# Kernel optimization log

Measured on AMD Instinct MI355X. Metric: run time of the kernel, lower is better.

Reference implementation:

```python
import jax, jax.numpy as jnp
import numpy as np

BL = 5           # block_len
BS = BL * BL     # block_size = 25
NH = 8           # num_heads
MASK_ONES = 12   # first 12 window positions unmasked (causal raster mask)


def _rel_pos_index():
    coords = np.stack(np.meshgrid(np.arange(BL), np.arange(BL), indexing='ij')).reshape(2, -1)
    rel = coords[:, :, None] - coords[:, None, :]          # [2, 25, 25]
    idx = (rel[0] + BL - 1) * (2 * BL - 1) + (rel[1] + BL - 1)
    return idx                                              # [25, 25] int

_REL_IDX = _rel_pos_index()


def _layernorm(x, w, b, eps=1e-5):
    m = jnp.mean(x, axis=-1, keepdims=True)
    v = jnp.var(x, axis=-1, keepdims=True)
    return (x - m) * jax.lax.rsqrt(v + eps) * w + b


def setup_inputs() -> dict:
    key = jax.random.key(0)
    ks = jax.random.split(key, 16)
    B, C, H, W = 4, 64, 64, 64
    out_dim = 64
    hidden = int(C * 4.0)
    s = lambda k, shape, scale=0.02: jax.random.normal(k, shape, dtype=jnp.float32) * scale
    return {
        'x': jax.random.normal(ks[0], (B, C, H, W), dtype=jnp.float32),
        'norm1_w': jnp.ones((C,), jnp.float32), 'norm1_b': jnp.zeros((C,), jnp.float32),
        'qkv_w': s(ks[1], (3 * C, C)), 'qkv_b': s(ks[2], (3 * C,)),
        'rpb_table': s(ks[3], ((2 * BL - 1) * (2 * BL - 1), NH)),
        'norm2_w': jnp.ones((C,), jnp.float32), 'norm2_b': jnp.zeros((C,), jnp.float32),
        'fc1_w': s(ks[4], (hidden, C)), 'fc1_b': s(ks[5], (hidden,)),
        'fc2_w': s(ks[6], (C, hidden)), 'fc2_b': s(ks[7], (C,)),
        'proj_w': s(ks[8], (out_dim, C)), 'proj_b': s(ks[9], (out_dim,)),
    }


def reference(x, norm1_w, norm1_b, qkv_w, qkv_b, rpb_table,
              norm2_w, norm2_b, fc1_w, fc1_b, fc2_w, fc2_b, proj_w, proj_b):
    B, C, H, W = x.shape
    hd = C // NH
    scale = hd ** (-0.5)

    # F.unfold(kernel=5, pad=2): per-pixel 5x5 neighborhood, channel-major then (kh,kw)
    xp = jnp.pad(x, ((0, 0), (0, 0), (2, 2), (2, 2)))
    patches = jnp.stack([xp[:, :, i:i + H, j:j + W] for i in range(BL) for j in range(BL)], axis=2)  # [B,C,25,H,W]
    x_unfold = patches.reshape(B, C, BS, H * W).transpose(0, 3, 2, 1)  # [B,HW,25,C]

    mask = (jnp.arange(BS) < MASK_ONES).astype(x.dtype)[None, None, :, None]
    x_masked = x_unfold * mask

    out = _layernorm(x_masked, norm1_w, norm1_b)
    qkv = out @ qkv_w.T + qkv_b                                 # [B,HW,25,3C]
    qkv = qkv.reshape(B, H * W, BS, 3, NH, hd).transpose(3, 0, 1, 4, 2, 5)  # [3,B,HW,nh,25,hd]
    q, k, v = qkv[0] * scale, qkv[1], qkv[2]

    attn = jnp.einsum('bpnqd,bpnkd->bpnqk', q, k)               # [B,HW,nh,25,25]
    bias = rpb_table[_REL_IDX.reshape(-1)].reshape(BS, BS, NH).transpose(2, 0, 1)  # [nh,25,25]
    attn = jax.nn.softmax(attn + bias[None, None], axis=-1)

    o = jnp.einsum('bpnqk,bpnkd->bpnqd', attn, v)               # [B,HW,nh,25,hd]
    o = o.transpose(0, 1, 3, 2, 4).reshape(B, H * W, BS, C)
    o = o + x_masked
    out_sumed = jnp.sum(o, axis=2)                              # [B,HW,C]

    y = _layernorm(out_sumed, norm2_w, norm2_b)
    y = jax.nn.gelu(y @ fc1_w.T + fc1_b, approximate=False) @ fc2_w.T + fc2_b
    y = y + out_sumed
    y = y @ proj_w.T + proj_b                                   # [B,HW,out_dim]
    return y.reshape(B, H, W, -1).transpose(0, 3, 1, 2)
```

## Files before the change

### kernel.cpp

```cpp
#include <hip/hip_runtime.h>
#include <hip/hip_bf16.h>


typedef _Float16 h2f __attribute__((ext_vector_type(2)));
typedef _Float16 h8  __attribute__((ext_vector_type(8)));
union u8h { h8 v; h2f p[4]; };
union pk4 { _Float16 h[4]; unsigned int u[2]; };

__device__ __forceinline__ float fdot2f(h2f a, h2f b, float c) {
#if defined(__has_builtin)
#if __has_builtin(__builtin_amdgcn_fdot2)
    return __builtin_amdgcn_fdot2(a, b, c, false);
#else
    return c + (float)a.x*(float)b.x + (float)a.y*(float)b.y;
#endif
#else
    return c + (float)a.x*(float)b.x + (float)a.y*(float)b.y;
#endif
}
__device__ __forceinline__ float dot8(u8h a, u8h b) {
    float c = 0.f;
    c = fdot2f(a.p[0], b.p[0], c);
    c = fdot2f(a.p[1], b.p[1], c);
    c = fdot2f(a.p[2], b.p[2], c);
    c = fdot2f(a.p[3], b.p[3], c);
    return c;
}
__device__ __forceinline__ float frcp(float x) {
#if defined(__has_builtin)
#if __has_builtin(__builtin_amdgcn_rcpf)
    return __builtin_amdgcn_rcpf(x);
#else
    return 1.0f/x;
#endif
#else
    return 1.0f/x;
#endif
}
__device__ __forceinline__ u8h ldh8(const _Float16* p) { u8h r; __builtin_memcpy(&r, p, 16); return r; }
__device__ __forceinline__ void st16(_Float16* d, const float4& v) { __builtin_memcpy(d, &v, 16); }
__device__ __forceinline__ float4 ld16(const _Float16* p) { float4 v; __builtin_memcpy(&v, p, 16); return v; }

#define SC 0.35355339059327373f

__global__ __launch_bounds__(1024) void k_qkv(
    const float* __restrict__ x, const float* __restrict__ n1w, const float* __restrict__ n1b,
    const float* __restrict__ qw, const float* __restrict__ qb, const float* __restrict__ rpb,
    const float* __restrict__ w1, const float* __restrict__ w2, const float* __restrict__ pw,
    _Float16* __restrict__ qkvh, _Float16* __restrict__ qkvc_h, _Float16* __restrict__ eb7,
    _Float16* __restrict__ w1h, _Float16* __restrict__ w2h, _Float16* __restrict__ pwh,
    float* __restrict__ osT)
{
    __shared__ float smem[10368];
    const int t = threadIdx.x, bid = blockIdx.x;
    if (bid < 256) {
        float* sXf = smem;
        _Float16* sOut = (_Float16*)(smem + 4160);
        const int p0 = bid*64;
        const int b = p0 >> 12, hw0 = p0 & 4095;
        for (int i = t; i < 4096; i += 1024) {
            int c = i >> 6, pp = i & 63;
            sXf[pp*65 + c] = x[(size_t)b*262144 + (size_t)c*4096 + hw0 + pp];
        }
        __syncthreads();
        const int pix = t & 63, g = t >> 6;
        float xr[64]; float s = 0.f, s2 = 0.f;
        #pragma unroll
        for (int c = 0; c < 64; ++c) { float v = sXf[pix*65 + c]; xr[c] = v; s += v; s2 += v*v; }
        float m = s*0.015625f;
        float rstd = rsqrtf(fmaxf(s2*0.015625f - m*m, 0.f) + 1e-5f);
        #pragma unroll
        for (int c = 0; c < 64; ++c) xr[c] = (xr[c] - m)*rstd*n1w[c] + n1b[c];
        #pragma unroll
        for (int i4 = 0; i4 < 12; i4 += 4) {
            const int o = g*12 + i4;
            const float* wr = qw + o*64;
            float a0 = qb[o], a1 = qb[o+1], a2 = qb[o+2], a3 = qb[o+3];
            #pragma unroll 16
            for (int c = 0; c < 64; ++c) {
                float xv = xr[c];
                a0 += xv*wr[c]; a1 += xv*wr[64+c]; a2 += xv*wr[128+c]; a3 += xv*wr[192+c];
            }
            pk4 pk;
            pk.h[0]=(_Float16)a0; pk.h[1]=(_Float16)a1; pk.h[2]=(_Float16)a2; pk.h[3]=(_Float16)a3;
            __builtin_memcpy(sOut + pix*194 + o, &pk, 8);
        }
        __syncthreads();
        for (int i = t; i < 1536; i += 1024) {
            int pp = i/24, d4 = i%24;
            ((float4*)qkvh)[(size_t)bid*1536 + i] = ld16(sOut + pp*194 + d4*8);
        }
        return;
    }
    if (bid < 512) {
        float* sxp = smem;
        const int plane = bid - 256;
        for (int i = t; i < 4624; i += 1024) sxp[i] = 0.f;
        __syncthreads();
        const float* xp = x + (size_t)plane*4096;
        for (int i = t; i < 4096; i += 1024) {
            int r = i >> 6, w = i & 63;
            sxp[(r + 2)*68 + (w + 2)] = xp[i];
        }
        __syncthreads();
        const int c = plane & 63, b = plane >> 6;
        float* op = osT + (size_t)c*16384 + b*4096;
        for (int i = t; i < 4096; i += 1024) {
            int r = i >> 6, w = i & 63;
            const float* s0 = sxp + r*68 + w;
            float sv = s0[0]+s0[1]+s0[2]+s0[3]+s0[4]
                     + s0[68]+s0[69]+s0[70]+s0[71]+s0[72]
                     + s0[136]+s0[137];
            op[i] = sv;
        }
        return;
    }
    if (bid < 520) {
        const int cid = bid - 512;
        for (int i = t; i < 4608; i += 1024) {
            int j = cid*4608 + i;
            if (j < 16384)      w1h[j]          = (_Float16)w1[j];
            else if (j < 32768) w2h[j - 16384]  = (_Float16)w2[j - 16384];
            else                pwh[j - 32768]  = (_Float16)pw[j - 32768];
        }
        return;
    }
    if (t < 192) {
        float acc = qb[t];
        for (int c = 0; c < 64; ++c) acc += n1b[c]*qw[t*64 + c];
        qkvc_h[t] = (_Float16)acc;
    }
    for (int i = t; i < 3200; i += 1024) {
        int j = i & 7, hf = (i >> 3) & 1, r = i >> 4;
        int h = r/25, q = r - h*25;
        float v = 0.f;
        if (j < 6) {
            int k = hf*6 + j;
            int ridx = (q/5 - k/5 + 4)*9 + (q%5 - k%5 + 4);
            v = __expf(rpb[ridx*8 + h]);
        } else if (j == 6 && hf) {
            for (int k = 12; k < 25; ++k) {
                int ridx = (q/5 - k/5 + 4)*9 + (q%5 - k%5 + 4);
                v += __expf(rpb[ridx*8 + h]);
            }
        }
        eb7[i] = (_Float16)v;
    }
}

__global__ __launch_bounds__(512) void k_fused(
    const _Float16* __restrict__ qkvh, const _Float16* __restrict__ qkvc_h,
    const _Float16* __restrict__ eb7g, const float* __restrict__ osT,
    const float* __restrict__ n2w, const float* __restrict__ n2b,
    const float* __restrict__ b1, const float* __restrict__ b2, const float* __restrict__ pb,
    const _Float16* __restrict__ w1h, const _Float16* __restrict__ w2h, const _Float16* __restrict__ pwh,
    float* __restrict__ out)
{
    __shared__ alignas(16) char smem[57040];
    _Float16* sq   = (_Float16*)(smem);
    _Float16* seb  = (_Float16*)(smem + 41920);
    _Float16* sqc  = (_Float16*)(smem + 48320);
    float*    sOs  = (float*)   (smem + 48704);
    _Float16* sH   = (_Float16*)(smem);
    h2f*      sAv  = (h2f*)     (smem + 16512);
    float*    sRW  = (float*)   (smem + 20880);
    float*    sMR  = (float*)   (smem + 23008);
    _Float16* sY   = (_Float16*)(smem + 41920);

    const int t = threadIdx.x;
    const int p0 = blockIdx.x*32;
    const int b = p0 >> 12, hw0 = p0 & 4095, hrow = hw0 >> 6, w0c = hw0 & 63;

    for (int i = t; i < 1600; i += 512) ((unsigned int*)seb)[i] = ((const unsigned int*)eb7g)[i];
    if (t < 96) ((unsigned int*)sqc)[t] = ((const unsigned int*)qkvc_h)[t];
    for (int i = t; i < 2592; i += 512) {
        int row = i/24, d4 = i%24;
        int rr = row/36, cc = row%36;
        int gr = hrow - 2 + rr, gc = w0c - 2 + cc;
        float4 v = (gr >= 0 && gc >= 0 && gc < 64)
            ? ((const float4*)qkvh)[(size_t)((b << 12) + (gr << 6) + gc)*24 + d4]
            : ((const float4*)qkvc_h)[d4];
        st16(sq + row*194 + d4*8, v);
    }
    for (int i = t; i < 2048; i += 512) {
        int c = i >> 5, pp = i & 31;
        sOs[pp*65 + c] = osT[(size_t)c*16384 + p0 + pp];
    }
    __syncthreads();

    {
        const int pix = t & 31, hf = (t >> 5) & 1, h = t >> 6, hb = h*8;
        int rws[6];
        #pragma unroll
        for (int j = 0; j < 6; ++j) { int k = hf*6 + j; rws[j] = (k/5)*36 + pix + (k%5); }
        u8h kreg[7];
        #pragma unroll
        for (int j = 0; j < 6; ++j) kreg[j] = ldh8(sq + rws[j]*194 + 64 + hb);
        kreg[6] = hf ? ldh8(sqc + 64 + hb) : kreg[0];
        u8h qcu = ldh8(sqc + hb);
        float edc[7];
        #pragma unroll
        for (int j = 0; j < 7; ++j) edc[j] = __expf(dot8(qcu, kreg[j])*SC);
        float w[7];
        #pragma unroll
        for (int j = 0; j < 7; ++j) w[j] = 0.f;
        const _Float16* ebbase = seb + h*400 + hf*8;

        for (int sIdx = 0; sIdx < 12; ++sIdx) {
            int rq = (sIdx/5)*36 + pix + (sIdx%5);
            u8h qu = ldh8(sq + rq*194 + hb);
            h8 eb8; __builtin_memcpy(&eb8, ebbase + sIdx*16, 16);
            float e[7]; float rs = 0.f;
            #pragma unroll
            for (int j = 0; j < 7; ++j) {
                float ev = __expf(dot8(qu, kreg[j])*SC)*(float)eb8[j];
                e[j] = ev; rs += ev;
            }
            rs += __shfl_xor(rs, 32);
            float inv = frcp(rs);
            #pragma unroll
            for (int j = 0; j < 7; ++j) w[j] += e[j]*inv;
        }
        for (int q = 12; q < 25; ++q) {
            h8 eb8; __builtin_memcpy(&eb8, ebbase + q*16, 16);
            float e[7]; float rs = 0.f;
            #pragma unroll
            for (int j = 0; j < 7; ++j) {
                float ev = edc[j]*(float)eb8[j];
                e[j] = ev; rs += ev;
            }
            rs += __shfl_xor(rs, 32);
            float inv = frcp(rs);
            #pragma unroll
            for (int j = 0; j < 7; ++j) w[j] += e[j]*inv;
        }
        float o8[8];
        #pragma unroll
        for (int d = 0; d < 8; ++d) o8[d] = 0.f;
        #pragma unroll
        for (int j = 0; j < 7; ++j) {
            const _Float16* vp = (j < 6) ? (sq + rws[j]*194 + 128 + hb)
                                         : (hf ? sqc + 128 + hb : sq + rws[0]*194 + 128 + hb);
            u8h vv = ldh8(vp);
            float wj = w[j];
            #pragma unroll
            for (int d4 = 0; d4 < 4; ++d4) {
                h2f pr = vv.p[d4];
                o8[d4*2]   += wj*(float)pr.x;
                o8[d4*2+1] += wj*(float)pr.y;
            }
        }
        #pragma unroll
        for (int d = 0; d < 8; ++d) o8[d] += __shfl_xor(o8[d], 32);
        const int c0 = hb + hf*4;
        float* ap = sOs + pix*65 + c0;
        #pragma unroll
        for (int j = 0; j < 4; ++j) ap[j] += o8[hf*4 + j];
    }
    __syncthreads();

    const int pix = t & 31, sl = t >> 5;
    const int c4 = sl*4;
    float ps = 0.f, ps2 = 0.f;
    float vch[4];
    #pragma unroll
    for (int j = 0; j < 4; ++j) {
        float v = sOs[pix*65 + c4 + j];
        vch[j] = v; ps += v; ps2 += v*v;
    }
    ps  += __shfl_xor(ps, 32);
    ps2 += __shfl_xor(ps2, 32);
    const int wv = t >> 6;
    if (((t >> 5) & 1) == 0) {
        sRW[(wv*33 + pix)*2]     = ps;
        sRW[(wv*33 + pix)*2 + 1] = ps2;
    }
    __syncthreads();
    if (t < 32) {
        float s = 0.f, s2 = 0.f;
        #pragma unroll
        for (int g = 0; g < 8; ++g) { s += sRW[(g*33 + t)*2]; s2 += sRW[(g*33 + t)*2 + 1]; }
        float m = s*0.015625f;
        sMR[t*2]     = m;
        sMR[t*2 + 1] = rsqrtf(fmaxf(s2*0.015625f - m*m, 0.f) + 1e-5f);
    }
    __syncthreads();
    {
        float m = sMR[pix*2], r = sMR[pix*2 + 1];
        #pragma unroll
        for (int j = 0; j < 2; ++j) {
            float e0 = (vch[2*j]   - m)*r*n2w[c4 + 2*j]   + n2b[c4 + 2*j];
            float e1 = (vch[2*j+1] - m)*r*n2w[c4 + 2*j+1] + n2b[c4 + 2*j+1];
            sAv[pix*34 + sl*2 + j] = h2f{(_Float16)e0, (_Float16)e1};
        }
    }
    __syncthreads();

    {
        const h2f* avr = sAv + pix*34;
        #pragma unroll
        for (int i4 = 0; i4 < 16; i4 += 4) {
            const int j = sl*16 + i4;
            const h2f* wr = (const h2f*)(w1h + (size_t)j*64);
            float a0 = b1[j], a1 = b1[j+1], a2 = b1[j+2], a3 = b1[j+3];
            #pragma unroll
            for (int cp = 0; cp < 32; ++cp) {
                h2f xv = avr[cp];
                a0 = fdot2f(xv, wr[cp],      a0);
                a1 = fdot2f(xv, wr[32 + cp], a1);
                a2 = fdot2f(xv, wr[64 + cp], a2);
                a3 = fdot2f(xv, wr[96 + cp], a3);
            }
            sH[pix*258 + j]     = (_Float16)(0.5f*a0*(1.f + erff(a0*0.70710678f)));
            sH[pix*258 + j + 1] = (_Float16)(0.5f*a1*(1.f + erff(a1*0.70710678f)));
            sH[pix*258 + j + 2] = (_Float16)(0.5f*a2*(1.f + erff(a2*0.70710678f)));
            sH[pix*258 + j + 3] = (_Float16)(0.5f*a3*(1.f + erff(a3*0.70710678f)));
        }
    }
    __syncthreads();

    {
        const int o = sl*4;
        const h2f* wr = (const h2f*)(w2h + (size_t)o*256);
        const h2f* hr = (const h2f*)(sH + pix*258);
        float a0 = b2[o], a1 = b2[o+1], a2 = b2[o+2], a3 = b2[o+3];
        #pragma unroll 32
        for (int jp = 0; jp < 128; ++jp) {
            h2f hv = hr[jp];
            a0 = fdot2f(hv, wr[jp],       a0);
            a1 = fdot2f(hv, wr[128 + jp], a1);
            a2 = fdot2f(hv, wr[256 + jp], a2);
            a3 = fdot2f(hv, wr[384 + jp], a3);
        }
        a0 += sOs[pix*65 + o];
        a1 += sOs[pix*65 + o + 1];
        a2 += sOs[pix*65 + o + 2];
        a3 += sOs[pix*65 + o + 3];
        sY[pix*74 + o]     = (_Float16)a0;
        sY[pix*74 + o + 1] = (_Float16)a1;
        sY[pix*74 + o + 2] = (_Float16)a2;
        sY[pix*74 + o + 3] = (_Float16)a3;
    }
    __syncthreads();

    {
        const int o = sl*4;
        const h2f* wr = (const h2f*)(pwh + (size_t)o*64);
        const h2f* yr = (const h2f*)(sY + pix*74);
        float a0 = pb[o], a1 = pb[o+1], a2 = pb[o+2], a3 = pb[o+3];
        #pragma unroll
        for (int cp = 0; cp < 32; ++cp) {
            h2f yv = yr[cp];
            a0 = fdot2f(yv, wr[cp],      a0);
            a1 = fdot2f(yv, wr[32 + cp], a1);
            a2 = fdot2f(yv, wr[64 + cp], a2);
            a3 = fdot2f(yv, wr[96 + cp], a3);
        }
        const int p = p0 + pix;
        const int bimg = p >> 12, hw = p & 4095, hh = hw >> 6, ww = hw & 63;
        float* ob = out + ((size_t)((bimg*64 + o)*64 + hh))*64 + ww;
        ob[0]     = a0;
        ob[4096]  = a1;
        ob[8192]  = a2;
        ob[12288] = a3;
    }
}

extern "C" void kernel_launch(void* const* d_in, const int* in_sizes, int n_in,
                              void* d_out, int out_size, void* d_ws, size_t ws_size,
                              hipStream_t stream) {
    const float* x   = (const float*)d_in[0];
    const float* n1w = (const float*)d_in[1];
    const float* n1b = (const float*)d_in[2];
    const float* qw  = (const float*)d_in[3];
    const float* qb  = (const float*)d_in[4];
    const float* rpb = (const float*)d_in[5];
    const float* n2w = (const float*)d_in[6];
    const float* n2b = (const float*)d_in[7];
    const float* w1  = (const float*)d_in[8];
    const float* b1  = (const float*)d_in[9];
    const float* w2  = (const float*)d_in[10];
    const float* b2  = (const float*)d_in[11];
    const float* pw  = (const float*)d_in[12];
    const float* pb  = (const float*)d_in[13];
    float* out = (float*)d_out;

    float* ws = (float*)d_ws;
    _Float16* qkvh   = (_Float16*)ws;
    float*    osT    = ws + 1572864;
    _Float16* qkvc_h = (_Float16*)(ws + 2621440);
    _Float16* eb7    = (_Float16*)(ws + 2621536);
    _Float16* w1h    = (_Float16*)(ws + 2623136);
    _Float16* w2h    = (_Float16*)(ws + 2631328);
    _Float16* pwh    = (_Float16*)(ws + 2639520);

    hipLaunchKernelGGL(k_qkv, dim3(521), dim3(1024), 0, stream,
                       x, n1w, n1b, qw, qb, rpb, w1, w2, pw,
                       qkvh, qkvc_h, eb7, w1h, w2h, pwh, osT);
    hipLaunchKernelGGL(k_fused, dim3(512), dim3(512), 0, stream,
                       qkvh, qkvc_h, eb7, osT,
                       n2w, n2b, b1, b2, pb, w1h, w2h, pwh, out);
}
```

Baseline: 215.0 us.

## Fuse masked window sum into attention kernel using fp16 x stored with qkv

The separate k_qkv blocks that built a padded plane and wrote the fp32 masked 5x5 window sum (osT) are removed. Instead, the QKV kernel appends the fp16 input channels to each pixel's qkv row, widening the row stride from 194 to 258. The fused kernel loads that halo into shared memory and computes the 12-tap window sum itself. This drops the osT write/read pass and about half the first-kernel grid, at the cost of wider qkv rows, more halo traffic, about 14 KB more LDS per block, and fp16 rounding of the residual input.

```diff
diff --git a/kernel.cpp b/kernel.cpp
--- a/kernel.cpp
+++ b/kernel.cpp
@@ -38,6 +38,7 @@
 #endif
 }
 __device__ __forceinline__ u8h ldh8(const _Float16* p) { u8h r; __builtin_memcpy(&r, p, 16); return r; }
+__device__ __forceinline__ h2f ldh2(const _Float16* p) { h2f r; __builtin_memcpy(&r, p, 4); return r; }
 __device__ __forceinline__ void st16(_Float16* d, const float4& v) { __builtin_memcpy(d, &v, 16); }
 __device__ __forceinline__ float4 ld16(const _Float16* p) { float4 v; __builtin_memcpy(&v, p, 16); return v; }
 
@@ -47,15 +48,13 @@
     const float* __restrict__ x, const float* __restrict__ n1w, const float* __restrict__ n1b,
     const float* __restrict__ qw, const float* __restrict__ qb, const float* __restrict__ rpb,
     const float* __restrict__ w1, const float* __restrict__ w2, const float* __restrict__ pw,
-    _Float16* __restrict__ qkvh, _Float16* __restrict__ qkvc_h, _Float16* __restrict__ eb7,
-    _Float16* __restrict__ w1h, _Float16* __restrict__ w2h, _Float16* __restrict__ pwh,
-    float* __restrict__ osT)
+    _Float16* __restrict__ qkvx, _Float16* __restrict__ qkvc_h, _Float16* __restrict__ eb7,
+    _Float16* __restrict__ w1h, _Float16* __restrict__ w2h, _Float16* __restrict__ pwh)
 {
-    __shared__ float smem[10368];
+    __shared__ float sXf[4160];
+    __shared__ alignas(16) _Float16 sOut[16512];
     const int t = threadIdx.x, bid = blockIdx.x;
     if (bid < 256) {
-        float* sXf = smem;
-        _Float16* sOut = (_Float16*)(smem + 4160);
         const int p0 = bid*64;
         const int b = p0 >> 12, hw0 = p0 & 4095;
         for (int i = t; i < 4096; i += 1024) {
@@ -63,6 +62,11 @@
             sXf[pp*65 + c] = x[(size_t)b*262144 + (size_t)c*4096 + hw0 + pp];
         }
         __syncthreads();
+        for (int i = t; i < 2048; i += 1024) {
+            int pp = i >> 5, j = i & 31;
+            h2f v = h2f{(_Float16)sXf[pp*65 + 2*j], (_Float16)sXf[pp*65 + 2*j + 1]};
+            __builtin_memcpy(sOut + pp*258 + 192 + 2*j, &v, 4);
+        }
         const int pix = t & 63, g = t >> 6;
         float xr[64]; float s = 0.f, s2 = 0.f;
         #pragma unroll
@@ -83,40 +87,17 @@
             }
             pk4 pk;
             pk.h[0]=(_Float16)a0; pk.h[1]=(_Float16)a1; pk.h[2]=(_Float16)a2; pk.h[3]=(_Float16)a3;
-            __builtin_memcpy(sOut + pix*194 + o, &pk, 8);
+            __builtin_memcpy(sOut + pix*258 + o, &pk, 8);
         }
         __syncthreads();
-        for (int i = t; i < 1536; i += 1024) {
-            int pp = i/24, d4 = i%24;
-            ((float4*)qkvh)[(size_t)bid*1536 + i] = ld16(sOut + pp*194 + d4*8);
+        for (int i = t; i < 2048; i += 1024) {
+            int pp = i >> 5, d4 = i & 31;
+            ((float4*)qkvx)[(size_t)bid*2048 + i] = ld16(sOut + pp*258 + d4*8);
         }
         return;
     }
-    if (bid < 512) {
-        float* sxp = smem;
-        const int plane = bid - 256;
-        for (int i = t; i < 4624; i += 1024) sxp[i] = 0.f;
-        __syncthreads();
-        const float* xp = x + (size_t)plane*4096;
-        for (int i = t; i < 4096; i += 1024) {
-            int r = i >> 6, w = i & 63;
-            sxp[(r + 2)*68 + (w + 2)] = xp[i];
-        }
-        __syncthreads();
-        const int c = plane & 63, b = plane >> 6;
-        float* op = osT + (size_t)c*16384 + b*4096;
-        for (int i = t; i < 4096; i += 1024) {
-            int r = i >> 6, w = i & 63;
-            const float* s0 = sxp + r*68 + w;
-            float sv = s0[0]+s0[1]+s0[2]+s0[3]+s0[4]
-                     + s0[68]+s0[69]+s0[70]+s0[71]+s0[72]
-                     + s0[136]+s0[137];
-            op[i] = sv;
-        }
-        return;
-    }
-    if (bid < 520) {
-        const int cid = bid - 512;
+    if (bid < 264) {
+        const int cid = bid - 256;
         for (int i = t; i < 4608; i += 1024) {
             int j = cid*4608 + i;
             if (j < 16384)      w1h[j]          = (_Float16)w1[j];
@@ -149,23 +130,23 @@
 }
 
 __global__ __launch_bounds__(512) void k_fused(
-    const _Float16* __restrict__ qkvh, const _Float16* __restrict__ qkvc_h,
-    const _Float16* __restrict__ eb7g, const float* __restrict__ osT,
+    const _Float16* __restrict__ qkvx, const _Float16* __restrict__ qkvc_h,
+    const _Float16* __restrict__ eb7g,
     const float* __restrict__ n2w, const float* __restrict__ n2b,
     const float* __restrict__ b1, const float* __restrict__ b2, const float* __restrict__ pb,
     const _Float16* __restrict__ w1h, const _Float16* __restrict__ w2h, const _Float16* __restrict__ pwh,
     float* __restrict__ out)
 {
-    __shared__ alignas(16) char smem[57040];
+    __shared__ alignas(16) char smem[70832];
     _Float16* sq   = (_Float16*)(smem);
-    _Float16* seb  = (_Float16*)(smem + 41920);
-    _Float16* sqc  = (_Float16*)(smem + 48320);
-    float*    sOs  = (float*)   (smem + 48704);
+    _Float16* seb  = (_Float16*)(smem + 55728);
+    _Float16* sqc  = (_Float16*)(smem + 62128);
+    float*    sOs  = (float*)   (smem + 62512);
     _Float16* sH   = (_Float16*)(smem);
     h2f*      sAv  = (h2f*)     (smem + 16512);
     float*    sRW  = (float*)   (smem + 20880);
     float*    sMR  = (float*)   (smem + 23008);
-    _Float16* sY   = (_Float16*)(smem + 41920);
+    _Float16* sY   = (_Float16*)(smem + 55728);
 
     const int t = threadIdx.x;
     const int p0 = blockIdx.x*32;
@@ -173,18 +154,35 @@
 
     for (int i = t; i < 1600; i += 512) ((unsigned int*)seb)[i] = ((const unsigned int*)eb7g)[i];
     if (t < 96) ((unsigned int*)sqc)[t] = ((const unsigned int*)qkvc_h)[t];
-    for (int i = t; i < 2592; i += 512) {
-        int row = i/24, d4 = i%24;
+    for (int i = t; i < 3456; i += 512) {
+        int row = i >> 5, d4 = i & 31;
         int rr = row/36, cc = row%36;
         int gr = hrow - 2 + rr, gc = w0c - 2 + cc;
-        float4 v = (gr >= 0 && gc >= 0 && gc < 64)
-            ? ((const float4*)qkvh)[(size_t)((b << 12) + (gr << 6) + gc)*24 + d4]
-            : ((const float4*)qkvc_h)[d4];
-        st16(sq + row*194 + d4*8, v);
-    }
-    for (int i = t; i < 2048; i += 512) {
-        int c = i >> 5, pp = i & 31;
-        sOs[pp*65 + c] = osT[(size_t)c*16384 + p0 + pp];
+        float4 v;
+        if (gr >= 0 && gc >= 0 && gc < 64)
+            v = ((const float4*)qkvx)[((size_t)((b << 12) + (gr << 6) + gc))*32 + d4];
+        else if (d4 < 24)
+            v = ((const float4*)qkvc_h)[d4];
+        else
+            v = make_float4(0.f, 0.f, 0.f, 0.f);
+        st16(sq + row*258 + d4*8, v);
+    }
+    __syncthreads();
+
+    {
+        const int pix = t & 31, sl = t >> 5;
+        const int c4 = sl*4;
+        float s0 = 0.f, s1 = 0.f, s2 = 0.f, s3 = 0.f;
+        #pragma unroll
+        for (int s = 0; s < 12; ++s) {
+            const _Float16* xp = sq + ((s/5)*36 + pix + (s%5))*258 + 192 + c4;
+            h2f a = ldh2(xp), bq = ldh2(xp + 2);
+            s0 += (float)a.x; s1 += (float)a.y; s2 += (float)bq.x; s3 += (float)bq.y;
+        }
+        sOs[pix*65 + c4]     = s0;
+        sOs[pix*65 + c4 + 1] = s1;
+        sOs[pix*65 + c4 + 2] = s2;
+        sOs[pix*65 + c4 + 3] = s3;
     }
     __syncthreads();
 
@@ -195,7 +193,7 @@
         for (int j = 0; j < 6; ++j) { int k = hf*6 + j; rws[j] = (k/5)*36 + pix + (k%5); }
         u8h kreg[7];
         #pragma unroll
-        for (int j = 0; j < 6; ++j) kreg[j] = ldh8(sq + rws[j]*194 + 64 + hb);
+        for (int j = 0; j < 6; ++j) kreg[j] = ldh8(sq + rws[j]*258 + 64 + hb);
         kreg[6] = hf ? ldh8(sqc + 64 + hb) : kreg[0];
         u8h qcu = ldh8(sqc + hb);
         float edc[7];
@@ -208,7 +206,7 @@
 
         for (int sIdx = 0; sIdx < 12; ++sIdx) {
             int rq = (sIdx/5)*36 + pix + (sIdx%5);
-            u8h qu = ldh8(sq + rq*194 + hb);
+            u8h qu = ldh8(sq + rq*258 + hb);
             h8 eb8; __builtin_memcpy(&eb8, ebbase + sIdx*16, 16);
             float e[7]; float rs = 0.f;
             #pragma unroll
@@ -239,8 +237,8 @@
         for (int d = 0; d < 8; ++d) o8[d] = 0.f;
         #pragma unroll
         for (int j = 0; j < 7; ++j) {
-            const _Float16* vp = (j < 6) ? (sq + rws[j]*194 + 128 + hb)
-                                         : (hf ? sqc + 128 + hb : sq + rws[0]*194 + 128 + hb);
+            const _Float16* vp = (j < 6) ? (sq + rws[j]*258 + 128 + hb)
+                                         : (hf ? sqc + 128 + hb : sq + rws[0]*258 + 128 + hb);
             u8h vv = ldh8(vp);
             float wj = w[j];
             #pragma unroll
@@ -386,18 +384,17 @@
     float* out = (float*)d_out;
 
     float* ws = (float*)d_ws;
-    _Float16* qkvh   = (_Float16*)ws;
-    float*    osT    = ws + 1572864;
-    _Float16* qkvc_h = (_Float16*)(ws + 2621440);
-    _Float16* eb7    = (_Float16*)(ws + 2621536);
-    _Float16* w1h    = (_Float16*)(ws + 2623136);
-    _Float16* w2h    = (_Float16*)(ws + 2631328);
-    _Float16* pwh    = (_Float16*)(ws + 2639520);
-
-    hipLaunchKernelGGL(k_qkv, dim3(521), dim3(1024), 0, stream,
+    _Float16* qkvx   = (_Float16*)ws;
+    _Float16* qkvc_h = (_Float16*)(ws + 2097152);
+    _Float16* eb7    = (_Float16*)(ws + 2097248);
+    _Float16* w1h    = (_Float16*)(ws + 2098848);
+    _Float16* w2h    = (_Float16*)(ws + 2107040);
+    _Float16* pwh    = (_Float16*)(ws + 2115232);
+
+    hipLaunchKernelGGL(k_qkv, dim3(265), dim3(1024), 0, stream,
                        x, n1w, n1b, qw, qb, rpb, w1, w2, pw,
-                       qkvh, qkvc_h, eb7, w1h, w2h, pwh, osT);
+                       qkvx, qkvc_h, eb7, w1h, w2h, pwh);
     hipLaunchKernelGGL(k_fused, dim3(512), dim3(512), 0, stream,
-                       qkvh, qkvc_h, eb7, osT,
+                       qkvx, qkvc_h, eb7,
                        n2w, n2b, b1, b2, pb, w1h, w2h, pwh, out);
 }
```

Result: no change. 212.2 us (-1.3%).
